# Optimization experiments

Hardware: AMD Instinct MI355X
Metric: run time of the kernel (lower is better)

The kernel has to match this reference:

```python
import math
import jax, jax.numpy as jnp
import numpy as np

G = 96       # grid side; N = G*G tokens, one token per grid cell
D = 512      # d_model
R = 2        # radius (Chebyshev)
LN_EPS = 1e-5

# 24 neighbor offsets in the (2R+1)^2 window, excluding (0,0) (self is excluded in the torch code)
_OFF = np.array([(dx, dy) for dx in range(-R, R + 1) for dy in range(-R, R + 1) if not (dx == 0 and dy == 0)], dtype=np.int32)


def _layer_norm(x, g, b):
    m = jnp.mean(x, axis=-1, keepdims=True)
    v = jnp.mean(jnp.square(x - m), axis=-1, keepdims=True)
    return (x - m) * jax.lax.rsqrt(v + LN_EPS) * g + b


def setup_inputs() -> dict:
    key = jax.random.key(0)
    ks = jax.random.split(key, 12)
    N = G * G
    x = jax.random.normal(ks[0], (N, D), jnp.float32)
    gx, gy = jnp.meshgrid(jnp.arange(G), jnp.arange(G), indexing='ij')
    grid = jnp.stack([gx.ravel(), gy.ravel()], axis=-1).astype(jnp.int32)  # [N,2], one token per cell

    def lin(k, din, dout):
        return jax.random.normal(k, (din, dout), jnp.float32) * (1.0 / math.sqrt(din))

    return {
        'x': x, 'grid': grid,
        'Wq': lin(ks[1], D, D), 'bq': jnp.zeros((D,), jnp.float32),
        'Wk': lin(ks[2], D, D), 'bk': jnp.zeros((D,), jnp.float32),
        'Wv': lin(ks[3], D, D), 'bv': jnp.zeros((D,), jnp.float32),
        'Wo': lin(ks[4], D, D), 'bo': jnp.zeros((D,), jnp.float32),
        'g1': jnp.ones((D,), jnp.float32), 'b1': jnp.zeros((D,), jnp.float32),
        'g2': jnp.ones((D,), jnp.float32), 'b2': jnp.zeros((D,), jnp.float32),
        'W1': lin(ks[5], D, 4 * D), 'bf1': jnp.zeros((4 * D,), jnp.float32),
        'W2': lin(ks[6], 4 * D, D), 'bf2': jnp.zeros((D,), jnp.float32),
    }


def reference(x, grid, Wq, bq, Wk, bk, Wv, bv, Wo, bo, g1, b1, g2, b2, W1, bf1, W2, bf2):
    # dropout is identity (eval mode)
    h = _layer_norm(x, g1, b1)
    q = h @ Wq + bq
    k = h @ Wk + bk
    v = h @ Wv + bv

    off = jnp.asarray(_OFF)                      # [K=24, 2]
    nx = grid[:, 0:1] + off[None, :, 0]          # [N, K]
    ny = grid[:, 1:2] + off[None, :, 1]
    valid = (nx >= 0) & (nx < G) & (ny >= 0) & (ny < G)
    idx = jnp.where(valid, nx * G + ny, 0)       # row-major cell -> token index

    k_nbr = k[idx]                               # [N, K, D]
    v_nbr = v[idx]                               # [N, K, D]
    scores = jnp.einsum('nd,nkd->nk', q, k_nbr) / math.sqrt(D)
    neg = jnp.finfo(scores.dtype).min
    scores = jnp.where(valid, scores, neg)
    attn = jax.nn.softmax(scores, axis=-1)       # every token has >=8 valid neighbors for G>R
    out = jnp.einsum('nk,nkd->nd', attn, v_nbr)  # [N, D]

    x = x + out @ Wo + bo
    h2 = _layer_norm(x, g2, b2)
    ffn = jax.nn.gelu(h2 @ W1 + bf1, approximate=False) @ W2 + bf2
    return x + ffn
```

## Files before the change

### kernel.cpp

```cpp
#include <hip/hip_runtime.h>

typedef unsigned short u16;
typedef unsigned int u32;
typedef __bf16 bf16x8 __attribute__((ext_vector_type(8)));
typedef float f32x4 __attribute__((ext_vector_type(4)));

#define GRID_G 96
#define DMODEL 512
#define NTOK (GRID_G * GRID_G)

__device__ __forceinline__ u16 f2bf(float f) {
  return __builtin_bit_cast(u16, (__bf16)f);
}
__device__ __forceinline__ void unpack8(uint4 u, float* f) {
  f[0] = __builtin_bit_cast(float, u.x << 16);
  f[1] = __builtin_bit_cast(float, u.x & 0xffff0000u);
  f[2] = __builtin_bit_cast(float, u.y << 16);
  f[3] = __builtin_bit_cast(float, u.y & 0xffff0000u);
  f[4] = __builtin_bit_cast(float, u.z << 16);
  f[5] = __builtin_bit_cast(float, u.z & 0xffff0000u);
  f[6] = __builtin_bit_cast(float, u.w << 16);
  f[7] = __builtin_bit_cast(float, u.w & 0xffff0000u);
}
__device__ __forceinline__ float gelu_fast(float x) {
  float y = 0.7978845608f * (x + 0.044715f * x * x * x);
  float a = fabsf(y);
  float e = __expf(-2.0f * a);
  float th = (1.0f - e) / (1.0f + e);
  th = __builtin_copysignf(th, y);
  return 0.5f * x * (1.0f + th);
}

__device__ __forceinline__ void tr_tile(const float* __restrict__ src,
                                        u16* __restrict__ dst, int R, int C,
                                        int bx, int by, float (*tile)[33]) {
  int tx = threadIdx.x & 31, ty = threadIdx.x >> 5;
#pragma unroll
  for (int i = 0; i < 4; ++i) {
    int r = ty + i * 8;
    tile[r][tx] = src[(size_t)(by * 32 + r) * C + (bx * 32 + tx)];
  }
  __syncthreads();
#pragma unroll
  for (int i = 0; i < 4; ++i) {
    int c = ty + i * 8;
    dst[(size_t)(bx * 32 + c) * R + (by * 32 + tx)] = f2bf(tile[tx][c]);
  }
}

__global__ __launch_bounds__(256) void k_prep(
    const float* __restrict__ Wq, const float* __restrict__ Wk,
    const float* __restrict__ Wv, const float* __restrict__ Wo,
    const float* __restrict__ W1, const float* __restrict__ W2,
    const float* __restrict__ bq, const float* __restrict__ bk,
    const float* __restrict__ bv, const float* __restrict__ x,
    const float* __restrict__ g1, const float* __restrict__ b1,
    u16* __restrict__ WQT, u16* __restrict__ WKT, u16* __restrict__ WVT,
    u16* __restrict__ WOT, u16* __restrict__ W1T, u16* __restrict__ W2T,
    float* __restrict__ BCAT, u16* __restrict__ H) {
  __shared__ float tile[32][33];
  const int b = blockIdx.x;
  if (b < 1024) {
    int z = b >> 8, sub = b & 255;
    const float* s = z == 0 ? Wq : z == 1 ? Wk : z == 2 ? Wv : Wo;
    u16* d = z == 0 ? WQT : z == 1 ? WKT : z == 2 ? WVT : WOT;
    tr_tile(s, d, 512, 512, sub & 15, sub >> 4, tile);
  } else if (b < 2048) {
    int idx = b - 1024;
    tr_tile(W1, W1T, 512, 2048, idx & 63, idx >> 6, tile);
  } else if (b < 3072) {
    int idx = b - 2048;
    tr_tile(W2, W2T, 2048, 512, idx & 15, idx >> 4, tile);
  } else if (b < 3078) {
    int i = (b - 3072) * 256 + threadIdx.x;
    if (i < 512) BCAT[i] = bq[i];
    else if (i < 1024) BCAT[i] = bk[i - 512];
    else if (i < 1536) BCAT[i] = bv[i - 1024];
  } else {
    int tid = threadIdx.x, wid = tid >> 6, lane = tid & 63;
    int row = (b - 3078) * 4 + wid;
    const float* xr = x + (size_t)row * DMODEL;
    float4 v0 = *(const float4*)(xr + lane * 4);
    float4 v1 = *(const float4*)(xr + 256 + lane * 4);
    float s = v0.x + v0.y + v0.z + v0.w + v1.x + v1.y + v1.z + v1.w;
    float sq = v0.x * v0.x + v0.y * v0.y + v0.z * v0.z + v0.w * v0.w +
               v1.x * v1.x + v1.y * v1.y + v1.z * v1.z + v1.w * v1.w;
#pragma unroll
    for (int m = 1; m < 64; m <<= 1) {
      s += __shfl_xor(s, m);
      sq += __shfl_xor(sq, m);
    }
    float mean = s * (1.0f / DMODEL);
    float rstd = rsqrtf(sq * (1.0f / DMODEL) - mean * mean + 1e-5f);
    float4 ga = *(const float4*)(g1 + lane * 4);
    float4 gb = *(const float4*)(g1 + 256 + lane * 4);
    float4 ba = *(const float4*)(b1 + lane * 4);
    float4 bb = *(const float4*)(b1 + 256 + lane * 4);
    ushort4 o0, o1;
    o0.x = f2bf((v0.x - mean) * rstd * ga.x + ba.x);
    o0.y = f2bf((v0.y - mean) * rstd * ga.y + ba.y);
    o0.z = f2bf((v0.z - mean) * rstd * ga.z + ba.z);
    o0.w = f2bf((v0.w - mean) * rstd * ga.w + ba.w);
    o1.x = f2bf((v1.x - mean) * rstd * gb.x + bb.x);
    o1.y = f2bf((v1.y - mean) * rstd * gb.y + bb.y);
    o1.z = f2bf((v1.z - mean) * rstd * gb.z + bb.z);
    o1.w = f2bf((v1.w - mean) * rstd * gb.w + bb.w);
    u16* op = H + (size_t)row * DMODEL;
    *(ushort4*)(op + lane * 4) = o0;
    *(ushort4*)(op + 256 + lane * 4) = o1;
  }
}

__global__ __launch_bounds__(256) void k_layernorm_bf16(
    const float* __restrict__ x, const float* __restrict__ g,
    const float* __restrict__ b, u16* __restrict__ out) {
  int tid = threadIdx.x, wid = tid >> 6, lane = tid & 63;
  int row = blockIdx.x * 4 + wid;
  const float* xr = x + (size_t)row * DMODEL;
  float4 v0 = *(const float4*)(xr + lane * 4);
  float4 v1 = *(const float4*)(xr + 256 + lane * 4);
  float s = v0.x + v0.y + v0.z + v0.w + v1.x + v1.y + v1.z + v1.w;
  float sq = v0.x * v0.x + v0.y * v0.y + v0.z * v0.z + v0.w * v0.w +
             v1.x * v1.x + v1.y * v1.y + v1.z * v1.z + v1.w * v1.w;
#pragma unroll
  for (int m = 1; m < 64; m <<= 1) {
    s += __shfl_xor(s, m);
    sq += __shfl_xor(sq, m);
  }
  float mean = s * (1.0f / DMODEL);
  float rstd = rsqrtf(sq * (1.0f / DMODEL) - mean * mean + 1e-5f);
  float4 ga = *(const float4*)(g + lane * 4);
  float4 gb = *(const float4*)(g + 256 + lane * 4);
  float4 ba = *(const float4*)(b + lane * 4);
  float4 bb = *(const float4*)(b + 256 + lane * 4);
  ushort4 o0, o1;
  o0.x = f2bf((v0.x - mean) * rstd * ga.x + ba.x);
  o0.y = f2bf((v0.y - mean) * rstd * ga.y + ba.y);
  o0.z = f2bf((v0.z - mean) * rstd * ga.z + ba.z);
  o0.w = f2bf((v0.w - mean) * rstd * ga.w + ba.w);
  o1.x = f2bf((v1.x - mean) * rstd * gb.x + bb.x);
  o1.y = f2bf((v1.y - mean) * rstd * gb.y + bb.y);
  o1.z = f2bf((v1.z - mean) * rstd * gb.z + bb.z);
  o1.w = f2bf((v1.w - mean) * rstd * gb.w + bb.w);
  u16* op = out + (size_t)row * DMODEL;
  *(ushort4*)(op + lane * 4) = o0;
  *(ushort4*)(op + 256 + lane * 4) = o1;
}

__global__ __launch_bounds__(256) void k_attn(
    const u16* __restrict__ q, const u16* __restrict__ kk,
    const u16* __restrict__ vv, const int* __restrict__ gpos,
    u16* __restrict__ out) {
  int tid = threadIdx.x, wid = tid >> 6, lane = tid & 63;
  int n = blockIdx.x * 4 + wid;
  int px = gpos[2 * n], py = gpos[2 * n + 1];
  float qf[8];
  unpack8(*(const uint4*)(q + (size_t)n * DMODEL + lane * 8), qf);
  float sc[24];
  int nid[24];
  bool ok[24];
#pragma unroll
  for (int j = 0; j < 24; ++j) {
    int jj = j < 12 ? j : j + 1;
    int dx = jj / 5 - 2, dy = jj % 5 - 2;
    int nx = px + dx, ny = py + dy;
    bool val = (nx >= 0) && (nx < GRID_G) && (ny >= 0) && (ny < GRID_G);
    int id = val ? nx * GRID_G + ny : 0;
    ok[j] = val;
    nid[j] = id;
    float kf[8];
    unpack8(*(const uint4*)(kk + (size_t)id * DMODEL + lane * 8), kf);
    float p = 0.f;
#pragma unroll
    for (int e = 0; e < 8; ++e) p += qf[e] * kf[e];
#pragma unroll
    for (int m = 1; m < 64; m <<= 1) p += __shfl_xor(p, m);
    sc[j] = p * 0.04419417382415922f;
  }
  float mx = -3.0e38f;
#pragma unroll
  for (int j = 0; j < 24; ++j)
    if (ok[j]) mx = fmaxf(mx, sc[j]);
  float wsum = 0.f, w[24];
#pragma unroll
  for (int j = 0; j < 24; ++j) {
    w[j] = ok[j] ? __expf(sc[j] - mx) : 0.f;
    wsum += w[j];
  }
  float inv = __builtin_amdgcn_rcpf(wsum);
  float acc[8] = {0, 0, 0, 0, 0, 0, 0, 0};
#pragma unroll
  for (int j = 0; j < 24; ++j) {
    float vf[8];
    unpack8(*(const uint4*)(vv + (size_t)nid[j] * DMODEL + lane * 8), vf);
    float wj = w[j];
#pragma unroll
    for (int e = 0; e < 8; ++e) acc[e] += wj * vf[e];
  }
  uint4 o;
  o.x = (u32)f2bf(acc[0] * inv) | ((u32)f2bf(acc[1] * inv) << 16);
  o.y = (u32)f2bf(acc[2] * inv) | ((u32)f2bf(acc[3] * inv) << 16);
  o.z = (u32)f2bf(acc[4] * inv) | ((u32)f2bf(acc[5] * inv) << 16);
  o.w = (u32)f2bf(acc[6] * inv) | ((u32)f2bf(acc[7] * inv) << 16);
  *(uint4*)(out + (size_t)n * DMODEL + lane * 8) = o;
}

#define BARR { __builtin_amdgcn_s_barrier(); __builtin_amdgcn_sched_barrier(0); }
#define WAIT8 asm volatile("s_waitcnt vmcnt(8)" ::: "memory");
#define WAIT0 asm volatile("s_waitcnt vmcnt(0)" ::: "memory");
#define LGKM0 asm volatile("s_waitcnt lgkmcnt(0)" ::: "memory");

template <int EPI>
__global__ __launch_bounds__(256, 2) void k_gemm(
    const u16* __restrict__ A, const u16* __restrict__ Bt,
    const float* __restrict__ bias, const float* __restrict__ res,
    float* __restrict__ outF, u16* __restrict__ outB,
    int M, int N, int K, int tiles_n) {
  __shared__ u16 lds[32768];
  const int t = threadIdx.x, wid = t >> 6, lane = t & 63;
  const int nwg = gridDim.x, bid = blockIdx.x;
  const int l = ((bid & 7) * (nwg >> 3)) + (bid >> 3);
  const int bM = (l / tiles_n) * 128, bN = (l % tiles_n) * 128;
  const int wr = wid >> 1, wc = wid & 1, lr = lane & 15, lg = lane >> 4;

  const int rs = lane >> 3;
  const int cl = (lane & 7) ^ rs;
  const u16* gA[4];
  const u16* gB[4];
  int dstL[4];
#pragma unroll
  for (int j = 0; j < 4; ++j) {
    int r = wid * 32 + j * 8 + rs;
    gA[j] = A + (size_t)(bM + r) * K + cl * 8;
    gB[j] = Bt + (size_t)(bN + r) * K + cl * 8;
    dstL[j] = wid * 2048 + j * 512;
  }

#define STAGE1(BUF, KOFF)                                                             \
  {                                                                                   \
    _Pragma("unroll") for (int j = 0; j < 4; ++j) {                                   \
      __builtin_amdgcn_global_load_lds(                                               \
          (const __attribute__((address_space(1))) void*)(gA[j] + (KOFF)),            \
          (__attribute__((address_space(3))) void*)(lds + (BUF)*16384 + dstL[j]),     \
          16, 0, 0);                                                                  \
      __builtin_amdgcn_global_load_lds(                                               \
          (const __attribute__((address_space(1))) void*)(gB[j] + (KOFF)),            \
          (__attribute__((address_space(3))) void*)(lds + (BUF)*16384 + 8192 + dstL[j]), \
          16, 0, 0);                                                                  \
    }                                                                                 \
  }

  const int offA0 = (wr * 64 + lr) * 64 + ((0 + lg) ^ (lr & 7)) * 8;
  const int offA1 = (wr * 64 + lr) * 64 + ((4 + lg) ^ (lr & 7)) * 8;
  const int offB0 = (wc * 64 + lr) * 64 + ((0 + lg) ^ (lr & 7)) * 8;
  const int offB1 = (wc * 64 + lr) * 64 + ((4 + lg) ^ (lr & 7)) * 8;

  f32x4 acc[4][4];
#pragma unroll
  for (int i = 0; i < 4; ++i)
#pragma unroll
    for (int j = 0; j < 4; ++j) acc[i][j] = (f32x4){0.f, 0.f, 0.f, 0.f};

#define COMPUTE1(BUF)                                                                 \
  {                                                                                   \
    _Pragma("unroll") for (int ks = 0; ks < 2; ++ks) {                                \
      const int oa = (BUF)*16384 + (ks ? offA1 : offA0);                              \
      const int ob = (BUF)*16384 + 8192 + (ks ? offB1 : offB0);                       \
      bf16x8 af[4], bfr[4];                                                           \
      _Pragma("unroll") for (int mt = 0; mt < 4; ++mt)                                \
          af[mt] = __builtin_bit_cast(bf16x8, *(const uint4*)(lds + oa + mt * 1024)); \
      _Pragma("unroll") for (int nt = 0; nt < 4; ++nt)                                \
          bfr[nt] = __builtin_bit_cast(bf16x8, *(const uint4*)(lds + ob + nt * 1024));\
      _Pragma("unroll") for (int mt = 0; mt < 4; ++mt)                                \
          _Pragma("unroll") for (int nt = 0; nt < 4; ++nt)                            \
              acc[mt][nt] = __builtin_amdgcn_mfma_f32_16x16x32_bf16(                  \
                  af[mt], bfr[nt], acc[mt][nt], 0, 0, 0);                             \
    }                                                                                 \
  }

  const int nk = K >> 6;
  STAGE1(0, 0);
  int koff = 64;
  for (int tt = 0; tt < nk; tt += 2) {
    if (tt + 1 < nk) { STAGE1(1, koff); WAIT8 } else { WAIT0 }
    BARR;
    COMPUTE1(0);
    BARR;
    if (tt + 2 < nk) { STAGE1(0, koff + 64); WAIT8 } else { WAIT0 }
    BARR;
    COMPUTE1(1);
    BARR;
    koff += 128;
  }
#undef STAGE1
#undef COMPUTE1

#pragma unroll
  for (int mt = 0; mt < 4; ++mt) {
#pragma unroll
    for (int nt = 0; nt < 4; ++nt) {
      int col = bN + wc * 64 + nt * 16 + lr;
      float bc = bias[col];
      int row0 = bM + wr * 64 + mt * 16 + lg * 4;
#pragma unroll
      for (int r = 0; r < 4; ++r) {
        float val = acc[mt][nt][r] + bc;
        size_t off = (size_t)(row0 + r) * N + col;
        if constexpr (EPI == 1) {
          outF[off] = res[off] + val;
        } else {
          outB[off] = f2bf(val);
        }
      }
    }
  }
}

template <int EPI, int KDIM>
__global__ __launch_bounds__(512, 4) void k_gemm_hi2(
    const u16* __restrict__ A, const u16* __restrict__ Bt,
    const float* __restrict__ bias, u16* __restrict__ outB,
    int N, int tiles_n) {
  __shared__ u16 lds[24576];
  const int t = threadIdx.x, w = t >> 6, lane = t & 63;
  const int nwg = gridDim.x, bid = blockIdx.x;
  const int l = ((bid & 7) * (nwg >> 3)) + (bid >> 3);
  const int bM = (l / tiles_n) * 256, bN = (l % tiles_n) * 128;
  const int wr = w >> 1, wc = w & 1, lr = lane & 15, lg = lane >> 4;

  const int rs = lane >> 3;
  const int cl = (lane & 7) ^ rs;
  const u16* pA = A + (size_t)(bM + w * 8 + rs) * KDIM + cl * 8;
  const u16* pB = Bt + (size_t)(bN + w * 8 + rs) * KDIM + cl * 8;
  const int dbase = w * 512;

  const int offA0 = (wr * 64 + lr) * 64 + ((0 + lg) ^ (lr & 7)) * 8;
  const int offA1 = (wr * 64 + lr) * 64 + ((4 + lg) ^ (lr & 7)) * 8;
  const int offB0 = 16384 + (wc * 64 + lr) * 64 + ((0 + lg) ^ (lr & 7)) * 8;
  const int offB1 = 16384 + (wc * 64 + lr) * 64 + ((4 + lg) ^ (lr & 7)) * 8;

  f32x4 acc[4][4];
#pragma unroll
  for (int i = 0; i < 4; ++i)
#pragma unroll
    for (int j = 0; j < 4; ++j) acc[i][j] = (f32x4){0.f, 0.f, 0.f, 0.f};

  constexpr int nk = KDIM >> 6;
  for (int tt = 0; tt < nk; ++tt) {
    const int koff = tt << 6;
#pragma unroll
    for (int j = 0; j < 4; ++j)
      __builtin_amdgcn_global_load_lds(
          (const __attribute__((address_space(1))) void*)(pA + (size_t)j * 64 * KDIM + koff),
          (__attribute__((address_space(3))) void*)(lds + j * 4096 + dbase), 16, 0, 0);
#pragma unroll
    for (int j = 0; j < 2; ++j)
      __builtin_amdgcn_global_load_lds(
          (const __attribute__((address_space(1))) void*)(pB + (size_t)j * 64 * KDIM + koff),
          (__attribute__((address_space(3))) void*)(lds + 16384 + j * 4096 + dbase), 16, 0, 0);
    WAIT0;
    BARR;
#pragma unroll
    for (int ks = 0; ks < 2; ++ks) {
      const int oa = ks ? offA1 : offA0;
      const int ob = ks ? offB1 : offB0;
      bf16x8 af[4], bfr[4];
#pragma unroll
      for (int mt = 0; mt < 4; ++mt)
        af[mt] = __builtin_bit_cast(bf16x8, *(const uint4*)(lds + oa + mt * 1024));
#pragma unroll
      for (int nt = 0; nt < 4; ++nt)
        bfr[nt] = __builtin_bit_cast(bf16x8, *(const uint4*)(lds + ob + nt * 1024));
#pragma unroll
      for (int mt = 0; mt < 4; ++mt)
#pragma unroll
        for (int nt = 0; nt < 4; ++nt)
          acc[mt][nt] = __builtin_amdgcn_mfma_f32_16x16x32_bf16(af[mt], bfr[nt], acc[mt][nt], 0, 0, 0);
    }
    LGKM0;
    BARR;
  }

#pragma unroll
  for (int mt = 0; mt < 4; ++mt) {
#pragma unroll
    for (int nt = 0; nt < 4; ++nt) {
      int col = bN + wc * 64 + nt * 16 + lr;
      float bc = bias[col];
      int row0 = bM + wr * 64 + mt * 16 + lg * 4;
#pragma unroll
      for (int r = 0; r < 4; ++r) {
        float val = acc[mt][nt][r] + bc;
        if constexpr (EPI == 2) {
          outB[(size_t)(row0 + r) * N + col] = f2bf(gelu_fast(val));
        } else {
          int seg = col >> 9;
          size_t off = (size_t)seg * ((size_t)NTOK * DMODEL) +
                       (size_t)(row0 + r) * DMODEL + (col & 511);
          outB[off] = f2bf(val);
        }
      }
    }
  }
}

extern "C" void kernel_launch(void* const* d_in, const int* in_sizes, int n_in,
                              void* d_out, int out_size, void* d_ws, size_t ws_size,
                              hipStream_t stream) {
  const float* x = (const float*)d_in[0];
  const int* gpos = (const int*)d_in[1];
  const float* Wq = (const float*)d_in[2];
  const float* bq = (const float*)d_in[3];
  const float* Wk = (const float*)d_in[4];
  const float* bk = (const float*)d_in[5];
  const float* Wv = (const float*)d_in[6];
  const float* bv = (const float*)d_in[7];
  const float* Wo = (const float*)d_in[8];
  const float* bo = (const float*)d_in[9];
  const float* g1 = (const float*)d_in[10];
  const float* b1 = (const float*)d_in[11];
  const float* g2 = (const float*)d_in[12];
  const float* b2 = (const float*)d_in[13];
  const float* W1 = (const float*)d_in[14];
  const float* bf1 = (const float*)d_in[15];
  const float* W2 = (const float*)d_in[16];
  const float* bf2 = (const float*)d_in[17];
  float* out = (float*)d_out;
  char* ws = (char*)d_ws;

  constexpr size_t SZ_W512 = (size_t)512 * 512 * 2;
  constexpr size_t SZ_W2048 = (size_t)512 * 2048 * 2;
  constexpr size_t SZ_ACT = (size_t)NTOK * 512 * 2;

  u16* WQT = (u16*)(ws + 0);
  u16* WKT = (u16*)(ws + SZ_W512);
  u16* WVT = (u16*)(ws + 2 * SZ_W512);
  u16* WOT = (u16*)(ws + 3 * SZ_W512);
  u16* W1T = (u16*)(ws + 4 * SZ_W512);
  u16* W2T = (u16*)(ws + 4 * SZ_W512 + SZ_W2048);
  float* BCAT = (float*)(ws + 4 * SZ_W512 + 2 * SZ_W2048);
  char* actbase = ws + 4 * SZ_W512 + 2 * SZ_W2048 + 6144;
  u16* H = (u16*)(actbase);
  u16* Q = (u16*)(actbase + SZ_ACT);
  u16* KB = (u16*)(actbase + 2 * SZ_ACT);
  u16* VB = (u16*)(actbase + 3 * SZ_ACT);
  u16* H2 = (u16*)(actbase + 4 * SZ_ACT);
  u16* U = (u16*)(actbase);

  k_prep<<<5382, 256, 0, stream>>>(Wq, Wk, Wv, Wo, W1, W2, bq, bk, bv, x, g1, b1,
                                   WQT, WKT, WVT, WOT, W1T, W2T, BCAT, H);

  k_gemm_hi2<3, 512><<<432, 512, 0, stream>>>(H, WQT, BCAT, Q, 1536, 12);

  k_attn<<<NTOK / 4, 256, 0, stream>>>(Q, KB, VB, gpos, H);

  k_gemm<1><<<288, 256, 0, stream>>>(H, WOT, bo, x, out, nullptr, NTOK, 512, 512, 4);

  k_layernorm_bf16<<<NTOK / 4, 256, 0, stream>>>(out, g2, b2, H2);

  k_gemm_hi2<2, 512><<<576, 512, 0, stream>>>(H2, W1T, bf1, U, 2048, 16);

  k_gemm<1><<<288, 256, 0, stream>>>(U, W2T, bf2, out, out, nullptr, NTOK, 512, 2048, 4);
}
```

Before: 156.1 us.

## Split-K the FFN down-projection with atomic accumulation into pre-biased residual

The final W2 GEMM (K=2048) is split into two K halves launched as 576 workgroups instead of 288, each atomically adding its partial result into the output. To make this work, the second layernorm kernel now also writes x + bf2 into the output buffer, so the GEMM epilogue needs neither bias nor a residual read. This is meant to improve occupancy and wave count on the long-K GEMM, at the cost of float atomics on the output, extra writes in the layernorm, and nondeterministic summation order.

```diff
diff --git a/kernel.cpp b/kernel.cpp
--- a/kernel.cpp
+++ b/kernel.cpp
@@ -113,7 +113,8 @@
 
 __global__ __launch_bounds__(256) void k_layernorm_bf16(
     const float* __restrict__ x, const float* __restrict__ g,
-    const float* __restrict__ b, u16* __restrict__ out) {
+    const float* __restrict__ b, u16* __restrict__ out,
+    float* __restrict__ yupd, const float* __restrict__ badd) {
   int tid = threadIdx.x, wid = tid >> 6, lane = tid & 63;
   int row = blockIdx.x * 4 + wid;
   const float* xr = x + (size_t)row * DMODEL;
@@ -145,6 +146,13 @@
   u16* op = out + (size_t)row * DMODEL;
   *(ushort4*)(op + lane * 4) = o0;
   *(ushort4*)(op + 256 + lane * 4) = o1;
+  float4 c0 = *(const float4*)(badd + lane * 4);
+  float4 c1 = *(const float4*)(badd + 256 + lane * 4);
+  float4 w0 = {v0.x + c0.x, v0.y + c0.y, v0.z + c0.z, v0.w + c0.w};
+  float4 w1 = {v1.x + c1.x, v1.y + c1.y, v1.z + c1.z, v1.w + c1.w};
+  float* yp = yupd + (size_t)row * DMODEL;
+  *(float4*)(yp + lane * 4) = w0;
+  *(float4*)(yp + 256 + lane * 4) = w1;
 }
 
 __global__ __launch_bounds__(256) void k_attn(
@@ -215,12 +223,20 @@
     const u16* __restrict__ A, const u16* __restrict__ Bt,
     const float* __restrict__ bias, const float* __restrict__ res,
     float* __restrict__ outF, u16* __restrict__ outB,
-    int M, int N, int K, int tiles_n) {
+    int M, int N, int K, int ldk, int tiles_n) {
   __shared__ u16 lds[32768];
   const int t = threadIdx.x, wid = t >> 6, lane = t & 63;
   const int nwg = gridDim.x, bid = blockIdx.x;
-  const int l = ((bid & 7) * (nwg >> 3)) + (bid >> 3);
+  const int l0 = ((bid & 7) * (nwg >> 3)) + (bid >> 3);
+  int l = l0, kh = 0;
+  if constexpr (EPI == 4) {
+    const int half = nwg >> 1;
+    kh = l0 >= half;
+    l = kh ? l0 - half : l0;
+  }
   const int bM = (l / tiles_n) * 128, bN = (l % tiles_n) * 128;
+  const u16* Ab = A + (size_t)kh * 1024;
+  const u16* Bb = Bt + (size_t)kh * 1024;
   const int wr = wid >> 1, wc = wid & 1, lr = lane & 15, lg = lane >> 4;
 
   const int rs = lane >> 3;
@@ -231,8 +247,8 @@
 #pragma unroll
   for (int j = 0; j < 4; ++j) {
     int r = wid * 32 + j * 8 + rs;
-    gA[j] = A + (size_t)(bM + r) * K + cl * 8;
-    gB[j] = Bt + (size_t)(bN + r) * K + cl * 8;
+    gA[j] = Ab + (size_t)(bM + r) * ldk + cl * 8;
+    gB[j] = Bb + (size_t)(bN + r) * ldk + cl * 8;
     dstL[j] = wid * 2048 + j * 512;
   }
 
@@ -300,7 +316,8 @@
 #pragma unroll
     for (int nt = 0; nt < 4; ++nt) {
       int col = bN + wc * 64 + nt * 16 + lr;
-      float bc = bias[col];
+      float bc = 0.f;
+      if constexpr (EPI != 4) bc = bias[col];
       int row0 = bM + wr * 64 + mt * 16 + lg * 4;
 #pragma unroll
       for (int r = 0; r < 4; ++r) {
@@ -308,6 +325,8 @@
         size_t off = (size_t)(row0 + r) * N + col;
         if constexpr (EPI == 1) {
           outF[off] = res[off] + val;
+        } else if constexpr (EPI == 4) {
+          atomicAdd(&outF[off], val);
         } else {
           outB[off] = f2bf(val);
         }
@@ -454,11 +473,12 @@
 
   k_attn<<<NTOK / 4, 256, 0, stream>>>(Q, KB, VB, gpos, H);
 
-  k_gemm<1><<<288, 256, 0, stream>>>(H, WOT, bo, x, out, nullptr, NTOK, 512, 512, 4);
-
-  k_layernorm_bf16<<<NTOK / 4, 256, 0, stream>>>(out, g2, b2, H2);
+  k_gemm<1><<<288, 256, 0, stream>>>(H, WOT, bo, x, out, nullptr, NTOK, 512, 512, 512, 4);
+
+  k_layernorm_bf16<<<NTOK / 4, 256, 0, stream>>>(out, g2, b2, H2, out, bf2);
 
   k_gemm_hi2<2, 512><<<576, 512, 0, stream>>>(H2, W1T, bf1, U, 2048, 16);
 
-  k_gemm<1><<<288, 256, 0, stream>>>(U, W2T, bf2, out, out, nullptr, NTOK, 512, 2048, 4);
-}
+  k_gemm<4><<<576, 256, 0, stream>>>(U, W2T, nullptr, nullptr, out, nullptr,
+                                     NTOK, 512, 1024, 2048, 4);
+}
```

After: 174.5 us. +11.7%, slower.
